# Kernel tuning notes

Hardware: AMD Instinct MI355X
Metric: run time of the kernel (lower is better)

Reference implementation:

```python
import jax, jax.numpy as jnp
import numpy as np


def setup_inputs() -> dict:
    key = jax.random.key(0)
    k1, k2, k3, k4, k5 = jax.random.split(key, 5)
    B, S, D, F, E = 4, 4096, 1024, 2048, 8
    top_k = 2
    num_tokens = B * S
    capacity = max(int(num_tokens / E * 1.25), 4)  # 2560
    scale = 0.02
    return {
        "x": jax.random.normal(k1, (B, S, D), dtype=jnp.float32),
        "gate_w": jax.random.normal(k2, (D, E), dtype=jnp.float32) * scale,
        "w_gate": jax.random.normal(k3, (E, D, F), dtype=jnp.float32) * scale,
        "w_up": jax.random.normal(k4, (E, D, F), dtype=jnp.float32) * scale,
        "w_down": jax.random.normal(k5, (E, F, D), dtype=jnp.float32) * scale,
        "num_experts": E,
        "top_k": top_k,
        "capacity": capacity,
    }


AUX_LOSS_WEIGHT = 0.01


def reference(x, gate_w, w_gate, w_up, w_down, num_experts, top_k, capacity):
    B, S, D = x.shape
    N = B * S
    x_flat = x.reshape(N, D)

    # ---- Router ----
    logits = x_flat @ gate_w                      # [N, E]
    probs = jax.nn.softmax(logits, axis=-1)
    weights, indices = jax.lax.top_k(probs, top_k)  # [N, K]
    weights = weights / jnp.sum(weights, axis=-1, keepdims=True)

    # ---- Capacity-based dispatch ----
    indices_flat = indices.reshape(-1)            # [N*K]
    x_rep = jnp.repeat(x_flat, top_k, axis=0)     # [N*K, D]
    expert_mask = jax.nn.one_hot(indices_flat, num_experts, dtype=jnp.int32)  # [N*K, E]
    token_priority = jnp.cumsum(expert_mask, axis=0) * expert_mask
    token_rank = jnp.sum(token_priority, axis=1)  # [N*K], 1-based rank within expert
    valid = (token_rank > 0) & (token_rank <= capacity)
    gather_idx = indices_flat * capacity + (token_rank - 1)  # [N*K]

    total_slots = num_experts * capacity
    # drop-mode scatter: invalid rows are sent out-of-bounds and dropped
    safe_idx = jnp.where(valid, gather_idx, total_slots)
    dispatched = jnp.zeros((total_slots, D), dtype=x.dtype)
    dispatched = dispatched.at[safe_idx].set(x_rep, mode="drop")
    dispatched = dispatched.reshape(num_experts, capacity, D)  # [E, C, D]

    # ---- Fused experts (grouped BMM, SwiGLU) ----
    gate = jnp.einsum("ecd,edf->ecf", dispatched, w_gate)
    up = jnp.einsum("ecd,edf->ecf", dispatched, w_up)
    hidden = jax.nn.silu(gate) * up
    expert_out = jnp.einsum("ecf,efd->ecd", hidden, w_down)
    expert_out_flat = expert_out.reshape(total_slots, D)

    # ---- Combine (row-aligned gather; dropped tokens contribute zero) ----
    gathered = expert_out_flat[jnp.clip(gather_idx, 0, total_slots - 1)]
    combined = jnp.where(valid[:, None], gathered, jnp.zeros((), dtype=x.dtype))
    combined = combined.reshape(N, top_k, D)
    output = jnp.sum(combined * weights[:, :, None], axis=1)  # [N, D]

    # ---- Aux load-balance loss ----
    mask = jax.nn.one_hot(indices, num_experts, dtype=jnp.float32).sum(axis=1)  # [N, E]
    f = mask.sum(axis=0) / (N * top_k + 1e-9)
    P = probs.mean(axis=0)
    aux_loss = num_experts * jnp.sum(f * P) * AUX_LOSS_WEIGHT

    return output.reshape(B, S, D), aux_loss
```

## Files before the change

kernel.cpp:

```cpp
#include <hip/hip_runtime.h>
#include <stdint.h>

#define N_TOK 16384
#define DIM   1024
#define NEXP  8
#define FF    2048
#define CAP   2560
#define NSLOT (NEXP*CAP)

using f32x4  = __attribute__((ext_vector_type(4))) float;
using bf16x8 = __attribute__((ext_vector_type(8))) short;

__device__ __forceinline__ unsigned short f2bf(float f){
  union { float f; unsigned u; } c; c.f = f;
  unsigned u = c.u + 0x7FFFu + ((c.u >> 16) & 1u);
  return (unsigned short)(u >> 16);
}
__device__ __forceinline__ float bf2f(unsigned short h){
  union { unsigned u; float f; } c; c.u = ((unsigned)h) << 16; return c.f;
}

__device__ __forceinline__ void gld16(const unsigned short* g, unsigned short* l){
  __builtin_amdgcn_global_load_lds((__attribute__((address_space(1))) void*)(void*)g,
                                   (__attribute__((address_space(3))) void*)l,
                                   16, 0, 0);
}

#define HBAR __builtin_amdgcn_s_barrier()
#define LG0  asm volatile("s_waitcnt lgkmcnt(0)" ::: "memory")

__global__ __launch_bounds__(256) void k_router(
    const float* __restrict__ x, const float* __restrict__ gate_w,
    float* __restrict__ probs, int* __restrict__ topidx, float* __restrict__ topw)
{
  __shared__ float gwT[NEXP][DIM];
  int tid = threadIdx.x;
  for (int i = tid; i < DIM*NEXP; i += 256) gwT[i & 7][i >> 3] = gate_w[i];
  __syncthreads();
  int wave = tid >> 6, lane = tid & 63;
  int t = blockIdx.x * 4 + wave;
  const float* xr = x + (size_t)t * DIM;
  double acc[NEXP];
  #pragma unroll
  for (int e = 0; e < NEXP; e++) acc[e] = 0.0;
  for (int j = 0; j < DIM/64; j++){
    double xv = (double)xr[lane + 64*j];
    #pragma unroll
    for (int e = 0; e < NEXP; e++) acc[e] += xv * (double)gwT[e][lane + 64*j];
  }
  #pragma unroll
  for (int off = 32; off >= 1; off >>= 1){
    #pragma unroll
    for (int e = 0; e < NEXP; e++) acc[e] += __shfl_xor(acc[e], off, 64);
  }
  if (lane == 0){
    double m = acc[0];
    #pragma unroll
    for (int e = 1; e < NEXP; e++) m = fmax(m, acc[e]);
    double p[NEXP], Z = 0.0;
    #pragma unroll
    for (int e = 0; e < NEXP; e++){ p[e] = exp(acc[e] - m); Z += p[e]; }
    double invZ = 1.0 / Z;
    #pragma unroll
    for (int e = 0; e < NEXP; e++){ p[e] *= invZ; probs[t*NEXP + e] = (float)p[e]; }
    int i0 = 0; double p0 = p[0];
    #pragma unroll
    for (int e = 1; e < NEXP; e++) if (p[e] > p0){ p0 = p[e]; i0 = e; }
    int i1 = (i0 == 0) ? 1 : 0; double p1 = p[i1];
    #pragma unroll
    for (int e = 0; e < NEXP; e++) if (e != i0 && p[e] > p1){ p1 = p[e]; i1 = e; }
    double s = p0 + p1;
    topidx[t*2+0] = i0; topidx[t*2+1] = i1;
    topw [t*2+0] = (float)(p0/s); topw[t*2+1] = (float)(p1/s);
  }
}

__global__ __launch_bounds__(1024) void k_scan(
    const int* __restrict__ topidx,
    int* __restrict__ slot_token, int* __restrict__ tok_slots,
    int* __restrict__ counts_total)
{
  __shared__ int sc[1024][NEXP];
  const int t = threadIdx.x;
  const int base_i = t * 32;
  int ids[32];
  #pragma unroll
  for (int j = 0; j < 32; j++) ids[j] = topidx[base_i + j];
  int b[NEXP];
  #pragma unroll
  for (int e = 0; e < NEXP; e++) b[e] = 0;
  #pragma unroll
  for (int j = 0; j < 32; j++){
    #pragma unroll
    for (int e = 0; e < NEXP; e++) if (ids[j] == e) b[e]++;
  }
  #pragma unroll
  for (int e = 0; e < NEXP; e++) sc[t][e] = b[e];
  __syncthreads();
  for (int off = 1; off < 1024; off <<= 1){
    int tmp[NEXP];
    #pragma unroll
    for (int e = 0; e < NEXP; e++) tmp[e] = (t >= off) ? sc[t-off][e] : 0;
    __syncthreads();
    #pragma unroll
    for (int e = 0; e < NEXP; e++) sc[t][e] += tmp[e];
    __syncthreads();
  }
  int myb[NEXP];
  #pragma unroll
  for (int e = 0; e < NEXP; e++) myb[e] = sc[t][e] - b[e];
  if (t == 1023){
    #pragma unroll
    for (int e = 0; e < NEXP; e++) counts_total[e] = sc[1023][e];
  }
  #pragma unroll
  for (int j = 0; j < 32; j++){
    int slot = -1;
    #pragma unroll
    for (int e = 0; e < NEXP; e++){
      if (ids[j] == e){
        int r = myb[e]; myb[e] = r + 1;
        if (r < CAP){
          slot = e*CAP + r;
          slot_token[slot] = (base_i + j) >> 1;
        }
      }
    }
    tok_slots[base_i + j] = slot;
  }
}

template<int MODE>
__global__ __launch_bounds__(256) void k_tcv(
    const float* __restrict__ in, unsigned short* __restrict__ out,
    int R, int C, size_t estride)
{
  __shared__ float tt[64][65];
  const int e  = blockIdx.z;
  const float* ine = in + (size_t)e * R * C;
  unsigned short* oute = out + (size_t)e * estride;
  const int c0 = blockIdx.x * 64, r0 = blockIdx.y * 64;
  const int tid = threadIdx.x;
  #pragma unroll
  for (int i = 0; i < 4; i++){
    int idx = i*256 + tid;
    int row = idx >> 4, c4 = idx & 15;
    float4 v = *(const float4*)(ine + (size_t)(r0 + row)*C + c0 + c4*4);
    tt[c4*4+0][row] = v.x; tt[c4*4+1][row] = v.y;
    tt[c4*4+2][row] = v.z; tt[c4*4+3][row] = v.w;
  }
  __syncthreads();
  #pragma unroll
  for (int i = 0; i < 2; i++){
    int cl = i*32 + (tid >> 3);
    int rs = (tid & 7) * 8;
    int c  = c0 + cl;
    int orow = (MODE == 0) ? ((c>>4)*32 + (c&15))
             : (MODE == 1) ? ((c>>4)*32 + 16 + (c&15))
             : c;
    unsigned long long pk0 = 0, pk1 = 0;
    #pragma unroll
    for (int j = 0; j < 4; j++) pk0 |= (unsigned long long)f2bf(tt[cl][rs+j]) << (16*j);
    #pragma unroll
    for (int j = 0; j < 4; j++) pk1 |= (unsigned long long)f2bf(tt[cl][rs+4+j]) << (16*j);
    unsigned long long* dst = (unsigned long long*)(oute + (size_t)orow*R + r0 + rs);
    dst[0] = pk0; dst[1] = pk1;
  }
}

__global__ __launch_bounds__(256) void k_gather(
    const float* __restrict__ x, const int* __restrict__ slot_token,
    unsigned short* __restrict__ disp)
{
  const int s = blockIdx.x;
  const int t = slot_token[s];
  const int tid = threadIdx.x;
  unsigned long long pk = 0ull;
  if (t >= 0){
    float4 v = *(const float4*)(x + (size_t)t*DIM + tid*4);
    pk =  (unsigned long long)f2bf(v.x)
       | ((unsigned long long)f2bf(v.y) << 16)
       | ((unsigned long long)f2bf(v.z) << 32)
       | ((unsigned long long)f2bf(v.w) << 48);
  }
  *(unsigned long long*)(disp + (size_t)s*DIM + tid*4) = pk;
}

__device__ __forceinline__ void stg(const unsigned short* gsrc, int ldg,
                                    unsigned short* Lh, int wave, int lane){
  const int sl = (lane & 3) ^ ((lane >> 3) & 3);
  #pragma unroll
  for (int j = 0; j < 2; j++){
    int bi = wave*2 + j;
    gld16(gsrc + (size_t)(bi*16 + (lane >> 2))*ldg + sl*8, Lh + bi*512);
  }
}
__device__ __forceinline__ bf16x8 frd(const unsigned short* Lh, int r, int g){
  return *(const bf16x8*)(Lh + r*32 + (((g ^ ((r >> 1) & 3))) << 3));
}
template<int MG>
__device__ __forceinline__ void mm16(f32x4 (&acc)[8][4], const bf16x8 (&a)[4], const bf16x8 (&b)[4]){
  #pragma unroll
  for (int i = 0; i < 4; i++)
    #pragma unroll
    for (int n = 0; n < 4; n++)
      acc[MG*4+i][n] = __builtin_amdgcn_mfma_f32_16x16x32_bf16(a[i], b[n], acc[MG*4+i][n], 0, 0, 0);
}

#define HALF_STEP(RS, DOSTG, VMW, ASRC, BSRC)                                   \
  {                                                                             \
    unsigned short* LA = lds + (RS)*16384;                                      \
    unsigned short* LB = LA + 8192;                                             \
    unsigned short* NS = lds + (((RS)+3)&3)*16384;                              \
    bf16x8 a[4], b[4];                                                          \
    _Pragma("unroll")                                                           \
    for (int i = 0; i < 4; i++) a[i] = frd(LA, wr*128 + i*16 + l15, g);         \
    _Pragma("unroll")                                                           \
    for (int n = 0; n < 4; n++) b[n] = frd(LB, wc*64 + n*16 + l15, g);          \
    if (DOSTG) stg(ASRC, KDIM, NS, wave, lane);                                 \
    HBAR; LG0;                                                                  \
    __builtin_amdgcn_s_setprio(1);  mm16<0>(acc, a, b);                         \
    __builtin_amdgcn_s_setprio(0);                                              \
    HBAR;                                                                       \
    _Pragma("unroll")                                                           \
    for (int i = 0; i < 4; i++) a[i] = frd(LA, wr*128 + (4+i)*16 + l15, g);     \
    if (DOSTG) stg(BSRC, KDIM, NS + 8192, wave, lane);                          \
    HBAR; LG0;                                                                  \
    __builtin_amdgcn_s_setprio(1);  mm16<1>(acc, a, b);                         \
    __builtin_amdgcn_s_setprio(0);                                              \
    if ((VMW) == 4) { asm volatile("s_waitcnt vmcnt(4)" ::: "memory"); }        \
    else if ((VMW) == 0) { asm volatile("s_waitcnt vmcnt(0)" ::: "memory"); }   \
    HBAR;                                                                       \
  }

template<int KDIM, int EPI>
__global__ __launch_bounds__(512, 2) void k_gemm8(
    const unsigned short* __restrict__ A,
    const unsigned short* __restrict__ B,
    unsigned short* __restrict__ Out)
{
  constexpr int NH    = KDIM / 32;
  constexpr int BROWS = (EPI == 1) ? 2*FF : DIM;
  constexpr int LDO   = (EPI == 1) ? FF : DIM;
  __shared__ unsigned short lds[65536];
  const int id = blockIdx.x;
  const int e  = id & 7;
  const int t  = id >> 3;
  const int mt = t % 10, nt = t / 10;
  const int m0 = mt*256, n0 = nt*256;
  const unsigned short* Ab = A + ((size_t)e*CAP   + m0) * KDIM;
  const unsigned short* Bb = B + ((size_t)e*BROWS + n0) * KDIM;
  const int tid = threadIdx.x, wave = tid >> 6, lane = tid & 63;
  const int wr = wave >> 2, wc = wave & 3;
  const int g = lane >> 4, l15 = lane & 15;

  f32x4 acc[8][4];
  const f32x4 z4 = {0.f,0.f,0.f,0.f};
  #pragma unroll
  for (int i = 0; i < 8; i++)
    #pragma unroll
    for (int n = 0; n < 4; n++) acc[i][n] = z4;

  stg(Ab,      KDIM, lds + 0*16384,        wave, lane);
  stg(Bb,      KDIM, lds + 0*16384 + 8192, wave, lane);
  stg(Ab + 32, KDIM, lds + 1*16384,        wave, lane);
  stg(Bb + 32, KDIM, lds + 1*16384 + 8192, wave, lane);
  stg(Ab + 64, KDIM, lds + 2*16384,        wave, lane);
  stg(Bb + 64, KDIM, lds + 2*16384 + 8192, wave, lane);
  asm volatile("s_waitcnt vmcnt(4)" ::: "memory");
  HBAR;

  for (int h = 0; h + 8 <= NH; h += 4){
    HALF_STEP(0, true, -1, Ab + (size_t)(h+3)*32, Bb + (size_t)(h+3)*32);
    HALF_STEP(1, true,  4, Ab + (size_t)(h+4)*32, Bb + (size_t)(h+4)*32);
    HALF_STEP(2, true, -1, Ab + (size_t)(h+5)*32, Bb + (size_t)(h+5)*32);
    HALF_STEP(3, true,  4, Ab + (size_t)(h+6)*32, Bb + (size_t)(h+6)*32);
  }
  HALF_STEP(0, true, -1, Ab + (size_t)(NH-1)*32, Bb + (size_t)(NH-1)*32);
  HALF_STEP(1, false, 0, Ab, Bb);
  HALF_STEP(2, false, -1, Ab, Bb);
  HALF_STEP(3, false, -1, Ab, Bb);

  if (EPI == 1){
    unsigned short* H = Out + ((size_t)e*CAP + m0 + wr*128) * (size_t)LDO;
    const int hc0 = (n0 + wc*64) >> 1;
    #pragma unroll
    for (int mf = 0; mf < 8; mf++)
      #pragma unroll
      for (int q = 0; q < 4; q++){
        int r = mf*16 + g*4 + q;
        #pragma unroll
        for (int p = 0; p < 2; p++){
          float gg = acc[mf][2*p][q], uu = acc[mf][2*p+1][q];
          float h = gg / (1.f + __expf(-gg)) * uu;
          H[(size_t)r*LDO + hc0 + p*16 + l15] = f2bf(h);
        }
      }
  } else {
    unsigned short* O = Out + ((size_t)e*CAP + m0 + wr*128) * (size_t)LDO + n0 + wc*64;
    #pragma unroll
    for (int mf = 0; mf < 8; mf++)
      #pragma unroll
      for (int q = 0; q < 4; q++){
        int r = mf*16 + g*4 + q;
        #pragma unroll
        for (int n = 0; n < 4; n++)
          O[(size_t)r*LDO + n*16 + l15] = f2bf(acc[mf][n][q]);
      }
  }
}

__global__ __launch_bounds__(256) void k_combine(
    const unsigned short* __restrict__ slot_out, const int* __restrict__ tok_slots,
    const float* __restrict__ topw, float* __restrict__ out)
{
  const int t = blockIdx.x*2 + (threadIdx.x >> 7);
  const int tid = threadIdx.x & 127;
  const int s0 = tok_slots[t*2+0], s1 = tok_slots[t*2+1];
  const float w0 = topw[t*2+0], w1 = topw[t*2+1];
  float r[8];
  #pragma unroll
  for (int j = 0; j < 8; j++) r[j] = 0.f;
  if (s0 >= 0){
    bf16x8 v = *(const bf16x8*)(slot_out + (size_t)s0*DIM + tid*8);
    #pragma unroll
    for (int j = 0; j < 8; j++) r[j] += w0 * bf2f((unsigned short)v[j]);
  }
  if (s1 >= 0){
    bf16x8 v = *(const bf16x8*)(slot_out + (size_t)s1*DIM + tid*8);
    #pragma unroll
    for (int j = 0; j < 8; j++) r[j] += w1 * bf2f((unsigned short)v[j]);
  }
  float4* o = (float4*)(out + (size_t)t*DIM + tid*8);
  o[0] = make_float4(r[0], r[1], r[2], r[3]);
  o[1] = make_float4(r[4], r[5], r[6], r[7]);
}

__global__ __launch_bounds__(256) void k_aux(
    const float* __restrict__ probs, const int* __restrict__ counts_total,
    float* __restrict__ aux_out)
{
  const int tid = threadIdx.x;
  float pe[NEXP];
  #pragma unroll
  for (int e = 0; e < NEXP; e++) pe[e] = 0.f;
  for (int i = tid; i < N_TOK; i += 256){
    #pragma unroll
    for (int e = 0; e < NEXP; e++) pe[e] += probs[i*NEXP + e];
  }
  #pragma unroll
  for (int off = 32; off >= 1; off >>= 1){
    #pragma unroll
    for (int e = 0; e < NEXP; e++) pe[e] += __shfl_xor(pe[e], off, 64);
  }
  __shared__ float part[4][NEXP];
  const int wave = tid >> 6, lane = tid & 63;
  if (lane == 0){
    #pragma unroll
    for (int e = 0; e < NEXP; e++) part[wave][e] = pe[e];
  }
  __syncthreads();
  if (tid == 0){
    float aux = 0.f;
    for (int e = 0; e < NEXP; e++){
      float P = (part[0][e] + part[1][e] + part[2][e] + part[3][e]) / (float)N_TOK;
      float f = (float)counts_total[e] / ((float)(N_TOK*2) + 1e-9f);
      aux += f * P;
    }
    aux_out[0] = (float)NEXP * aux * 0.01f;
  }
}

extern "C" void kernel_launch(void* const* d_in, const int* in_sizes, int n_in,
                              void* d_out, int out_size, void* d_ws, size_t ws_size,
                              hipStream_t stream)
{
  const float* x      = (const float*)d_in[0];
  const float* gate_w = (const float*)d_in[1];
  const float* w_gate = (const float*)d_in[2];
  const float* w_up   = (const float*)d_in[3];
  const float* w_down = (const float*)d_in[4];
  float* out = (float*)d_out;

  uint8_t* ws = (uint8_t*)d_ws;
  float* probs        = (float*)ws;             ws += (size_t)N_TOK*NEXP*4;
  int*   topidx       = (int*)ws;               ws += (size_t)N_TOK*2*4;
  float* topw         = (float*)ws;             ws += (size_t)N_TOK*2*4;
  int*   slot_token   = (int*)ws;               ws += (size_t)NSLOT*4;
  int*   tok_slots    = (int*)ws;               ws += (size_t)N_TOK*2*4;
  int*   counts_total = (int*)ws;               ws += 256;
  unsigned short* disp   = (unsigned short*)ws; ws += (size_t)NSLOT*DIM*2;
  unsigned short* hidden = (unsigned short*)ws; ws += (size_t)NSLOT*FF*2;
  unsigned short* B1     = (unsigned short*)ws; ws += (size_t)NEXP*2*FF*DIM*2;
  unsigned short* wdT    = (unsigned short*)ws; ws += (size_t)NEXP*DIM*FF*2;
  size_t need = (size_t)(ws - (uint8_t*)d_ws);
  if (ws_size < need) return;
  unsigned short* slot_out = disp;

  hipMemsetAsync(slot_token, 0xFF, (size_t)NSLOT * sizeof(int), stream);

  k_router<<<N_TOK/4, 256, 0, stream>>>(x, gate_w, probs, topidx, topw);
  k_scan<<<1, 1024, 0, stream>>>(topidx, slot_token, tok_slots, counts_total);
  k_tcv<0><<<dim3(FF/64, DIM/64, NEXP), 256, 0, stream>>>(w_gate, B1, DIM, FF, (size_t)2*FF*DIM);
  k_tcv<1><<<dim3(FF/64, DIM/64, NEXP), 256, 0, stream>>>(w_up,   B1, DIM, FF, (size_t)2*FF*DIM);
  k_tcv<2><<<dim3(DIM/64, FF/64, NEXP), 256, 0, stream>>>(w_down, wdT, FF, DIM, (size_t)DIM*FF);
  k_gather<<<NSLOT, 256, 0, stream>>>(x, slot_token, disp);
  k_gemm8<DIM, 1><<<1280, 512, 0, stream>>>(disp, B1, hidden);
  k_gemm8<FF, 2><<<320, 512, 0, stream>>>(hidden, wdT, slot_out);
  k_combine<<<N_TOK/2, 256, 0, stream>>>(slot_out, tok_slots, topw, out);
  k_aux<<<1, 256, 0, stream>>>(probs, counts_total, out + (size_t)N_TOK*DIM);
}
```

Baseline: 508.8 us.

## Split GEMM kernels; shrink LDS pipeline and use smaller tiles for down projection

```diff
diff --git a/kernel.cpp b/kernel.cpp
--- a/kernel.cpp
+++ b/kernel.cpp
@@ -28,6 +28,7 @@
 
 #define HBAR __builtin_amdgcn_s_barrier()
 #define LG0  asm volatile("s_waitcnt lgkmcnt(0)" ::: "memory")
+#define VM0  asm volatile("s_waitcnt vmcnt(0)" ::: "memory")
 
 __global__ __launch_bounds__(256) void k_router(
     const float* __restrict__ x, const float* __restrict__ gate_w,
@@ -207,49 +208,20 @@
       acc[MG*4+i][n] = __builtin_amdgcn_mfma_f32_16x16x32_bf16(a[i], b[n], acc[MG*4+i][n], 0, 0, 0);
 }
 
-#define HALF_STEP(RS, DOSTG, VMW, ASRC, BSRC)                                   \
-  {                                                                             \
-    unsigned short* LA = lds + (RS)*16384;                                      \
-    unsigned short* LB = LA + 8192;                                             \
-    unsigned short* NS = lds + (((RS)+3)&3)*16384;                              \
-    bf16x8 a[4], b[4];                                                          \
-    _Pragma("unroll")                                                           \
-    for (int i = 0; i < 4; i++) a[i] = frd(LA, wr*128 + i*16 + l15, g);         \
-    _Pragma("unroll")                                                           \
-    for (int n = 0; n < 4; n++) b[n] = frd(LB, wc*64 + n*16 + l15, g);          \
-    if (DOSTG) stg(ASRC, KDIM, NS, wave, lane);                                 \
-    HBAR; LG0;                                                                  \
-    __builtin_amdgcn_s_setprio(1);  mm16<0>(acc, a, b);                         \
-    __builtin_amdgcn_s_setprio(0);                                              \
-    HBAR;                                                                       \
-    _Pragma("unroll")                                                           \
-    for (int i = 0; i < 4; i++) a[i] = frd(LA, wr*128 + (4+i)*16 + l15, g);     \
-    if (DOSTG) stg(BSRC, KDIM, NS + 8192, wave, lane);                          \
-    HBAR; LG0;                                                                  \
-    __builtin_amdgcn_s_setprio(1);  mm16<1>(acc, a, b);                         \
-    __builtin_amdgcn_s_setprio(0);                                              \
-    if ((VMW) == 4) { asm volatile("s_waitcnt vmcnt(4)" ::: "memory"); }        \
-    else if ((VMW) == 0) { asm volatile("s_waitcnt vmcnt(0)" ::: "memory"); }   \
-    HBAR;                                                                       \
-  }
-
-template<int KDIM, int EPI>
-__global__ __launch_bounds__(512, 2) void k_gemm8(
+__global__ __launch_bounds__(512, 4) void k_gemm1(
     const unsigned short* __restrict__ A,
     const unsigned short* __restrict__ B,
     unsigned short* __restrict__ Out)
 {
-  constexpr int NH    = KDIM / 32;
-  constexpr int BROWS = (EPI == 1) ? 2*FF : DIM;
-  constexpr int LDO   = (EPI == 1) ? FF : DIM;
-  __shared__ unsigned short lds[65536];
+  constexpr int KDIM = DIM, NH = DIM/32;
+  __shared__ unsigned short lds[32768];
   const int id = blockIdx.x;
   const int e  = id & 7;
   const int t  = id >> 3;
   const int mt = t % 10, nt = t / 10;
   const int m0 = mt*256, n0 = nt*256;
-  const unsigned short* Ab = A + ((size_t)e*CAP   + m0) * KDIM;
-  const unsigned short* Bb = B + ((size_t)e*BROWS + n0) * KDIM;
+  const unsigned short* Ab = A + ((size_t)e*CAP  + m0) * KDIM;
+  const unsigned short* Bb = B + ((size_t)e*2*FF + n0) * KDIM;
   const int tid = threadIdx.x, wave = tid >> 6, lane = tid & 63;
   const int wr = wave >> 2, wc = wave & 3;
   const int g = lane >> 4, l15 = lane & 15;
@@ -261,53 +233,114 @@
     #pragma unroll
     for (int n = 0; n < 4; n++) acc[i][n] = z4;
 
-  stg(Ab,      KDIM, lds + 0*16384,        wave, lane);
-  stg(Bb,      KDIM, lds + 0*16384 + 8192, wave, lane);
-  stg(Ab + 32, KDIM, lds + 1*16384,        wave, lane);
-  stg(Bb + 32, KDIM, lds + 1*16384 + 8192, wave, lane);
-  stg(Ab + 64, KDIM, lds + 2*16384,        wave, lane);
-  stg(Bb + 64, KDIM, lds + 2*16384 + 8192, wave, lane);
-  asm volatile("s_waitcnt vmcnt(4)" ::: "memory");
-  HBAR;
-
-  for (int h = 0; h + 8 <= NH; h += 4){
-    HALF_STEP(0, true, -1, Ab + (size_t)(h+3)*32, Bb + (size_t)(h+3)*32);
-    HALF_STEP(1, true,  4, Ab + (size_t)(h+4)*32, Bb + (size_t)(h+4)*32);
-    HALF_STEP(2, true, -1, Ab + (size_t)(h+5)*32, Bb + (size_t)(h+5)*32);
-    HALF_STEP(3, true,  4, Ab + (size_t)(h+6)*32, Bb + (size_t)(h+6)*32);
-  }
-  HALF_STEP(0, true, -1, Ab + (size_t)(NH-1)*32, Bb + (size_t)(NH-1)*32);
-  HALF_STEP(1, false, 0, Ab, Bb);
-  HALF_STEP(2, false, -1, Ab, Bb);
-  HALF_STEP(3, false, -1, Ab, Bb);
-
-  if (EPI == 1){
-    unsigned short* H = Out + ((size_t)e*CAP + m0 + wr*128) * (size_t)LDO;
-    const int hc0 = (n0 + wc*64) >> 1;
-    #pragma unroll
-    for (int mf = 0; mf < 8; mf++)
+  stg(Ab, KDIM, lds,        wave, lane);
+  stg(Bb, KDIM, lds + 8192, wave, lane);
+  VM0; HBAR;
+
+  for (int h = 0; h < NH; ++h){
+    unsigned short* LA = lds + (h & 1)*16384;
+    unsigned short* LB = LA + 8192;
+    unsigned short* NS = lds + ((h & 1)^1)*16384;
+    const bool st = (h + 1 < NH);
+    bf16x8 a[4], b[4];
+    #pragma unroll
+    for (int i = 0; i < 4; i++) a[i] = frd(LA, wr*128 + i*16 + l15, g);
+    #pragma unroll
+    for (int n = 0; n < 4; n++) b[n] = frd(LB, wc*64 + n*16 + l15, g);
+    if (st) stg(Ab + (size_t)(h+1)*32, KDIM, NS, wave, lane);
+    HBAR; LG0;
+    __builtin_amdgcn_s_setprio(1);  mm16<0>(acc, a, b);  __builtin_amdgcn_s_setprio(0);
+    HBAR;
+    #pragma unroll
+    for (int i = 0; i < 4; i++) a[i] = frd(LA, wr*128 + (4+i)*16 + l15, g);
+    if (st) stg(Bb + (size_t)(h+1)*32, KDIM, NS + 8192, wave, lane);
+    HBAR; LG0;
+    __builtin_amdgcn_s_setprio(1);  mm16<1>(acc, a, b);  __builtin_amdgcn_s_setprio(0);
+    if (st) VM0;
+    HBAR;
+  }
+
+  unsigned short* H = Out + ((size_t)e*CAP + m0 + wr*128) * (size_t)FF;
+  const int hc0 = (n0 + wc*64) >> 1;
+  #pragma unroll
+  for (int mf = 0; mf < 8; mf++)
+    #pragma unroll
+    for (int q = 0; q < 4; q++){
+      int r = mf*16 + g*4 + q;
       #pragma unroll
-      for (int q = 0; q < 4; q++){
-        int r = mf*16 + g*4 + q;
-        #pragma unroll
-        for (int p = 0; p < 2; p++){
-          float gg = acc[mf][2*p][q], uu = acc[mf][2*p+1][q];
-          float h = gg / (1.f + __expf(-gg)) * uu;
-          H[(size_t)r*LDO + hc0 + p*16 + l15] = f2bf(h);
-        }
+      for (int p = 0; p < 2; p++){
+        float gg = acc[mf][2*p][q], uu = acc[mf][2*p+1][q];
+        float h = gg / (1.f + __expf(-gg)) * uu;
+        H[(size_t)r*FF + hc0 + p*16 + l15] = f2bf(h);
       }
-  } else {
-    unsigned short* O = Out + ((size_t)e*CAP + m0 + wr*128) * (size_t)LDO + n0 + wc*64;
-    #pragma unroll
-    for (int mf = 0; mf < 8; mf++)
+    }
+}
+
+__global__ __launch_bounds__(256, 4) void k_gemm2s(
+    const unsigned short* __restrict__ A,
+    const unsigned short* __restrict__ B,
+    unsigned short* __restrict__ Out)
+{
+  constexpr int KDIM = FF, NH = FF/32;
+  __shared__ unsigned short lds[16384];
+  const int id = blockIdx.x;
+  const int e  = id & 7;
+  const int t  = id >> 3;
+  const int mt = t % 20, nt = t / 20;
+  const int m0 = mt*128, n0 = nt*128;
+  const unsigned short* Ab = A + ((size_t)e*CAP + m0) * KDIM;
+  const unsigned short* Bb = B + ((size_t)e*DIM + n0) * KDIM;
+  const int tid = threadIdx.x, wave = tid >> 6, lane = tid & 63;
+  const int wr = wave >> 1, wc = wave & 1;
+  const int g = lane >> 4, l15 = lane & 15;
+
+  f32x4 acc[4][4];
+  const f32x4 z4 = {0.f,0.f,0.f,0.f};
+  #pragma unroll
+  for (int i = 0; i < 4; i++)
+    #pragma unroll
+    for (int n = 0; n < 4; n++) acc[i][n] = z4;
+
+  stg(Ab, KDIM, lds,        wave, lane);
+  stg(Bb, KDIM, lds + 4096, wave, lane);
+  VM0; HBAR;
+
+  for (int h = 0; h < NH; ++h){
+    unsigned short* LA = lds + (h & 1)*8192;
+    unsigned short* LB = LA + 4096;
+    unsigned short* NS = lds + ((h & 1)^1)*8192;
+    const bool st = (h + 1 < NH);
+    bf16x8 a[4], b[4];
+    #pragma unroll
+    for (int i = 0; i < 4; i++) a[i] = frd(LA, wr*64 + i*16 + l15, g);
+    #pragma unroll
+    for (int n = 0; n < 4; n++) b[n] = frd(LB, wc*64 + n*16 + l15, g);
+    if (st){
+      stg(Ab + (size_t)(h+1)*32, KDIM, NS,        wave, lane);
+      stg(Bb + (size_t)(h+1)*32, KDIM, NS + 4096, wave, lane);
+    }
+    HBAR; LG0;
+    __builtin_amdgcn_s_setprio(1);
+    #pragma unroll
+    for (int i = 0; i < 4; i++)
       #pragma unroll
-      for (int q = 0; q < 4; q++){
-        int r = mf*16 + g*4 + q;
-        #pragma unroll
-        for (int n = 0; n < 4; n++)
-          O[(size_t)r*LDO + n*16 + l15] = f2bf(acc[mf][n][q]);
-      }
-  }
+      for (int n = 0; n < 4; n++)
+        acc[i][n] = __builtin_amdgcn_mfma_f32_16x16x32_bf16(a[i], b[n], acc[i][n], 0, 0, 0);
+    __builtin_amdgcn_s_setprio(0);
+    if (st) VM0;
+    HBAR;
+  }
+
+  unsigned short* O = Out + ((size_t)e*CAP + m0 + wr*64) * (size_t)DIM + n0 + wc*64;
+  #pragma unroll
+  for (int mf = 0; mf < 4; mf++)
+    #pragma unroll
+    for (int q = 0; q < 4; q++){
+      int r = mf*16 + g*4 + q;
+      #pragma unroll
+      for (int n = 0; n < 4; n++)
+        O[(size_t)r*DIM + n*16 + l15] = f2bf(acc[mf][n][q]);
+    }
 }
 
 __global__ __launch_bounds__(256) void k_combine(
@@ -405,8 +438,8 @@
   k_tcv<1><<<dim3(FF/64, DIM/64, NEXP), 256, 0, stream>>>(w_up,   B1, DIM, FF, (size_t)2*FF*DIM);
   k_tcv<2><<<dim3(DIM/64, FF/64, NEXP), 256, 0, stream>>>(w_down, wdT, FF, DIM, (size_t)DIM*FF);
   k_gather<<<NSLOT, 256, 0, stream>>>(x, slot_token, disp);
-  k_gemm8<DIM, 1><<<1280, 512, 0, stream>>>(disp, B1, hidden);
-  k_gemm8<FF, 2><<<320, 512, 0, stream>>>(hidden, wdT, slot_out);
+  k_gemm1<<<1280, 512, 0, stream>>>(disp, B1, hidden);
+  k_gemm2s<<<1280, 256, 0, stream>>>(hidden, wdT, slot_out);
   k_combine<<<N_TOK/2, 256, 0, stream>>>(slot_out, tok_slots, topw, out);
   k_aux<<<1, 256, 0, stream>>>(probs, counts_total, out + (size_t)N_TOK*DIM);
 }
```

After: 2.032 ms. 299% more time.

## Split-K the down-projection GEMM into two partials summed in combine

Applied to the files above, without the earlier changes.

```diff
diff --git a/kernel.cpp b/kernel.cpp
--- a/kernel.cpp
+++ b/kernel.cpp
@@ -217,14 +217,14 @@
     for (int i = 0; i < 4; i++) a[i] = frd(LA, wr*128 + i*16 + l15, g);         \
     _Pragma("unroll")                                                           \
     for (int n = 0; n < 4; n++) b[n] = frd(LB, wc*64 + n*16 + l15, g);          \
-    if (DOSTG) stg(ASRC, KDIM, NS, wave, lane);                                 \
+    if (DOSTG) stg(ASRC, LDG, NS, wave, lane);                                  \
     HBAR; LG0;                                                                  \
     __builtin_amdgcn_s_setprio(1);  mm16<0>(acc, a, b);                         \
     __builtin_amdgcn_s_setprio(0);                                              \
     HBAR;                                                                       \
     _Pragma("unroll")                                                           \
     for (int i = 0; i < 4; i++) a[i] = frd(LA, wr*128 + (4+i)*16 + l15, g);     \
-    if (DOSTG) stg(BSRC, KDIM, NS + 8192, wave, lane);                          \
+    if (DOSTG) stg(BSRC, LDG, NS + 8192, wave, lane);                           \
     HBAR; LG0;                                                                  \
     __builtin_amdgcn_s_setprio(1);  mm16<1>(acc, a, b);                         \
     __builtin_amdgcn_s_setprio(0);                                              \
@@ -233,11 +233,12 @@
     HBAR;                                                                       \
   }
 
-template<int KDIM, int EPI>
+template<int KDIM, int LDG, int EPI>
 __global__ __launch_bounds__(512, 2) void k_gemm8(
     const unsigned short* __restrict__ A,
     const unsigned short* __restrict__ B,
-    unsigned short* __restrict__ Out)
+    unsigned short* __restrict__ Out0,
+    unsigned short* __restrict__ Out1)
 {
   constexpr int NH    = KDIM / 32;
   constexpr int BROWS = (EPI == 1) ? 2*FF : DIM;
@@ -245,11 +246,13 @@
   __shared__ unsigned short lds[65536];
   const int id = blockIdx.x;
   const int e  = id & 7;
-  const int t  = id >> 3;
+  int t  = id >> 3;
+  int ks = 0;
+  if (EPI == 2){ ks = t & 1; t >>= 1; }
   const int mt = t % 10, nt = t / 10;
   const int m0 = mt*256, n0 = nt*256;
-  const unsigned short* Ab = A + ((size_t)e*CAP   + m0) * KDIM;
-  const unsigned short* Bb = B + ((size_t)e*BROWS + n0) * KDIM;
+  const unsigned short* Ab = A + ((size_t)e*CAP   + m0) * LDG + (size_t)ks*KDIM;
+  const unsigned short* Bb = B + ((size_t)e*BROWS + n0) * LDG + (size_t)ks*KDIM;
   const int tid = threadIdx.x, wave = tid >> 6, lane = tid & 63;
   const int wr = wave >> 2, wc = wave & 3;
   const int g = lane >> 4, l15 = lane & 15;
@@ -261,12 +264,12 @@
     #pragma unroll
     for (int n = 0; n < 4; n++) acc[i][n] = z4;
 
-  stg(Ab,      KDIM, lds + 0*16384,        wave, lane);
-  stg(Bb,      KDIM, lds + 0*16384 + 8192, wave, lane);
-  stg(Ab + 32, KDIM, lds + 1*16384,        wave, lane);
-  stg(Bb + 32, KDIM, lds + 1*16384 + 8192, wave, lane);
-  stg(Ab + 64, KDIM, lds + 2*16384,        wave, lane);
-  stg(Bb + 64, KDIM, lds + 2*16384 + 8192, wave, lane);
+  stg(Ab,      LDG, lds + 0*16384,        wave, lane);
+  stg(Bb,      LDG, lds + 0*16384 + 8192, wave, lane);
+  stg(Ab + 32, LDG, lds + 1*16384,        wave, lane);
+  stg(Bb + 32, LDG, lds + 1*16384 + 8192, wave, lane);
+  stg(Ab + 64, LDG, lds + 2*16384,        wave, lane);
+  stg(Bb + 64, LDG, lds + 2*16384 + 8192, wave, lane);
   asm volatile("s_waitcnt vmcnt(4)" ::: "memory");
   HBAR;
 
@@ -282,7 +285,7 @@
   HALF_STEP(3, false, -1, Ab, Bb);
 
   if (EPI == 1){
-    unsigned short* H = Out + ((size_t)e*CAP + m0 + wr*128) * (size_t)LDO;
+    unsigned short* H = Out0 + ((size_t)e*CAP + m0 + wr*128) * (size_t)LDO;
     const int hc0 = (n0 + wc*64) >> 1;
     #pragma unroll
     for (int mf = 0; mf < 8; mf++)
@@ -297,7 +300,8 @@
         }
       }
   } else {
-    unsigned short* O = Out + ((size_t)e*CAP + m0 + wr*128) * (size_t)LDO + n0 + wc*64;
+    unsigned short* P = (ks ? Out1 : Out0);
+    unsigned short* O = P + ((size_t)e*CAP + m0 + wr*128) * (size_t)LDO + n0 + wc*64;
     #pragma unroll
     for (int mf = 0; mf < 8; mf++)
       #pragma unroll
@@ -311,8 +315,9 @@
 }
 
 __global__ __launch_bounds__(256) void k_combine(
-    const unsigned short* __restrict__ slot_out, const int* __restrict__ tok_slots,
-    const float* __restrict__ topw, float* __restrict__ out)
+    const unsigned short* __restrict__ P0, const unsigned short* __restrict__ P1,
+    const int* __restrict__ tok_slots, const float* __restrict__ topw,
+    float* __restrict__ out)
 {
   const int t = blockIdx.x*2 + (threadIdx.x >> 7);
   const int tid = threadIdx.x & 127;
@@ -322,14 +327,18 @@
   #pragma unroll
   for (int j = 0; j < 8; j++) r[j] = 0.f;
   if (s0 >= 0){
-    bf16x8 v = *(const bf16x8*)(slot_out + (size_t)s0*DIM + tid*8);
-    #pragma unroll
-    for (int j = 0; j < 8; j++) r[j] += w0 * bf2f((unsigned short)v[j]);
+    bf16x8 v0 = *(const bf16x8*)(P0 + (size_t)s0*DIM + tid*8);
+    bf16x8 v1 = *(const bf16x8*)(P1 + (size_t)s0*DIM + tid*8);
+    #pragma unroll
+    for (int j = 0; j < 8; j++)
+      r[j] += w0 * (bf2f((unsigned short)v0[j]) + bf2f((unsigned short)v1[j]));
   }
   if (s1 >= 0){
-    bf16x8 v = *(const bf16x8*)(slot_out + (size_t)s1*DIM + tid*8);
-    #pragma unroll
-    for (int j = 0; j < 8; j++) r[j] += w1 * bf2f((unsigned short)v[j]);
+    bf16x8 v0 = *(const bf16x8*)(P0 + (size_t)s1*DIM + tid*8);
+    bf16x8 v1 = *(const bf16x8*)(P1 + (size_t)s1*DIM + tid*8);
+    #pragma unroll
+    for (int j = 0; j < 8; j++)
+      r[j] += w1 * (bf2f((unsigned short)v0[j]) + bf2f((unsigned short)v1[j]));
   }
   float4* o = (float4*)(out + (size_t)t*DIM + tid*8);
   o[0] = make_float4(r[0], r[1], r[2], r[3]);
@@ -395,7 +404,8 @@
   unsigned short* wdT    = (unsigned short*)ws; ws += (size_t)NEXP*DIM*FF*2;
   size_t need = (size_t)(ws - (uint8_t*)d_ws);
   if (ws_size < need) return;
-  unsigned short* slot_out = disp;
+  unsigned short* P0 = disp;
+  unsigned short* P1 = B1;
 
   hipMemsetAsync(slot_token, 0xFF, (size_t)NSLOT * sizeof(int), stream);
 
@@ -405,8 +415,8 @@
   k_tcv<1><<<dim3(FF/64, DIM/64, NEXP), 256, 0, stream>>>(w_up,   B1, DIM, FF, (size_t)2*FF*DIM);
   k_tcv<2><<<dim3(DIM/64, FF/64, NEXP), 256, 0, stream>>>(w_down, wdT, FF, DIM, (size_t)DIM*FF);
   k_gather<<<NSLOT, 256, 0, stream>>>(x, slot_token, disp);
-  k_gemm8<DIM, 1><<<1280, 512, 0, stream>>>(disp, B1, hidden);
-  k_gemm8<FF, 2><<<320, 512, 0, stream>>>(hidden, wdT, slot_out);
-  k_combine<<<N_TOK/2, 256, 0, stream>>>(slot_out, tok_slots, topw, out);
+  k_gemm8<DIM, DIM, 1><<<1280, 512, 0, stream>>>(disp, B1, hidden, nullptr);
+  k_gemm8<DIM, FF, 2><<<640, 512, 0, stream>>>(hidden, wdT, P0, P1);
+  k_combine<<<N_TOK/2, 256, 0, stream>>>(P0, P1, tok_slots, topw, out);
   k_aux<<<1, 256, 0, stream>>>(probs, counts_total, out + (size_t)N_TOK*DIM);
 }
```

Result: no change. 501.6 us (-1.4%).

## Split down-projection GEMM into a narrower-tile kernel with its own pipeline

Applied to the files above, without the earlier changes.

```diff
diff --git a/kernel.cpp b/kernel.cpp
--- a/kernel.cpp
+++ b/kernel.cpp
@@ -28,6 +28,7 @@
 
 #define HBAR __builtin_amdgcn_s_barrier()
 #define LG0  asm volatile("s_waitcnt lgkmcnt(0)" ::: "memory")
+#define SBAR0 __builtin_amdgcn_sched_barrier(0)
 
 __global__ __launch_bounds__(256) void k_router(
     const float* __restrict__ x, const float* __restrict__ gate_w,
@@ -233,23 +234,20 @@
     HBAR;                                                                       \
   }
 
-template<int KDIM, int EPI>
-__global__ __launch_bounds__(512, 2) void k_gemm8(
+__global__ __launch_bounds__(512, 2) void k_gemm1(
     const unsigned short* __restrict__ A,
     const unsigned short* __restrict__ B,
     unsigned short* __restrict__ Out)
 {
-  constexpr int NH    = KDIM / 32;
-  constexpr int BROWS = (EPI == 1) ? 2*FF : DIM;
-  constexpr int LDO   = (EPI == 1) ? FF : DIM;
+  constexpr int KDIM = DIM, NH = DIM/32;
   __shared__ unsigned short lds[65536];
   const int id = blockIdx.x;
   const int e  = id & 7;
   const int t  = id >> 3;
   const int mt = t % 10, nt = t / 10;
   const int m0 = mt*256, n0 = nt*256;
-  const unsigned short* Ab = A + ((size_t)e*CAP   + m0) * KDIM;
-  const unsigned short* Bb = B + ((size_t)e*BROWS + n0) * KDIM;
+  const unsigned short* Ab = A + ((size_t)e*CAP  + m0) * KDIM;
+  const unsigned short* Bb = B + ((size_t)e*2*FF + n0) * KDIM;
   const int tid = threadIdx.x, wave = tid >> 6, lane = tid & 63;
   const int wr = wave >> 2, wc = wave & 3;
   const int g = lane >> 4, l15 = lane & 15;
@@ -281,33 +279,103 @@
   HALF_STEP(2, false, -1, Ab, Bb);
   HALF_STEP(3, false, -1, Ab, Bb);
 
-  if (EPI == 1){
-    unsigned short* H = Out + ((size_t)e*CAP + m0 + wr*128) * (size_t)LDO;
-    const int hc0 = (n0 + wc*64) >> 1;
-    #pragma unroll
-    for (int mf = 0; mf < 8; mf++)
+  unsigned short* H = Out + ((size_t)e*CAP + m0 + wr*128) * (size_t)FF;
+  const int hc0 = (n0 + wc*64) >> 1;
+  #pragma unroll
+  for (int mf = 0; mf < 8; mf++)
+    #pragma unroll
+    for (int q = 0; q < 4; q++){
+      int r = mf*16 + g*4 + q;
       #pragma unroll
-      for (int q = 0; q < 4; q++){
-        int r = mf*16 + g*4 + q;
-        #pragma unroll
-        for (int p = 0; p < 2; p++){
-          float gg = acc[mf][2*p][q], uu = acc[mf][2*p+1][q];
-          float h = gg / (1.f + __expf(-gg)) * uu;
-          H[(size_t)r*LDO + hc0 + p*16 + l15] = f2bf(h);
-        }
+      for (int p = 0; p < 2; p++){
+        float gg = acc[mf][2*p][q], uu = acc[mf][2*p+1][q];
+        float h = gg / (1.f + __expf(-gg)) * uu;
+        H[(size_t)r*FF + hc0 + p*16 + l15] = f2bf(h);
       }
-  } else {
-    unsigned short* O = Out + ((size_t)e*CAP + m0 + wr*128) * (size_t)LDO + n0 + wc*64;
-    #pragma unroll
-    for (int mf = 0; mf < 8; mf++)
+    }
+}
+
+__global__ __launch_bounds__(512, 2) void k_gemm2t(
+    const unsigned short* __restrict__ A,
+    const unsigned short* __restrict__ B,
+    unsigned short* __restrict__ Out)
+{
+  constexpr int KDIM = FF, NH = FF/32;
+  constexpr int SLOT = 12288;
+  __shared__ unsigned short lds[4*SLOT];
+  const int id = blockIdx.x;
+  const int e  = id & 7;
+  const int t  = id >> 3;
+  const int mt = t % 10, nt = t / 10;
+  const int m0 = mt*256, n0 = nt*128;
+  const unsigned short* Ab = A + ((size_t)e*CAP + m0) * KDIM;
+  const unsigned short* Bb = B + ((size_t)e*DIM + n0) * KDIM;
+  const int tid = threadIdx.x, wave = tid >> 6, lane = tid & 63;
+  const int wr = wave >> 2, wc = wave & 3;
+  const int g = lane >> 4, l15 = lane & 15;
+  const int sl = (lane & 3) ^ ((lane >> 3) & 3);
+
+  f32x4 acc[8][2];
+  const f32x4 z4 = {0.f,0.f,0.f,0.f};
+  #pragma unroll
+  for (int i = 0; i < 8; i++)
+    #pragma unroll
+    for (int n = 0; n < 2; n++) acc[i][n] = z4;
+
+  auto stage = [&](int h, int rs){
+    unsigned short* S = lds + rs*SLOT;
+    const unsigned short* As = Ab + (size_t)h*32;
+    const unsigned short* Bs = Bb + (size_t)h*32;
+    #pragma unroll
+    for (int j = 0; j < 2; j++){
+      int bi = wave*2 + j;
+      gld16(As + (size_t)(bi*16 + (lane >> 2))*KDIM + sl*8, S + bi*512);
+    }
+    gld16(Bs + (size_t)(wave*16 + (lane >> 2))*KDIM + sl*8, S + 8192 + wave*512);
+  };
+
+  stage(0,0); stage(1,1); stage(2,2);
+
+  for (int h = 0; h < NH; ++h){
+    if (h < NH-2)      { asm volatile("s_waitcnt vmcnt(6)" ::: "memory"); }
+    else if (h == NH-2){ asm volatile("s_waitcnt vmcnt(3)" ::: "memory"); }
+    else               { asm volatile("s_waitcnt vmcnt(0)" ::: "memory"); }
+    HBAR;
+    SBAR0;
+    unsigned short* LA = lds + (h & 3)*SLOT;
+    unsigned short* LB = LA + 8192;
+    if (h + 3 < NH) stage(h+3, (h+3) & 3);
+    bf16x8 a[4], a2[4], b[2];
+    #pragma unroll
+    for (int i = 0; i < 4; i++) a[i]  = frd(LA, wr*128 + i*16 + l15, g);
+    #pragma unroll
+    for (int n = 0; n < 2; n++) b[n]  = frd(LB, wc*32 + n*16 + l15, g);
+    #pragma unroll
+    for (int i = 0; i < 4; i++) a2[i] = frd(LA, wr*128 + (4+i)*16 + l15, g);
+    __builtin_amdgcn_s_setprio(1);
+    #pragma unroll
+    for (int i = 0; i < 4; i++)
       #pragma unroll
-      for (int q = 0; q < 4; q++){
-        int r = mf*16 + g*4 + q;
-        #pragma unroll
-        for (int n = 0; n < 4; n++)
-          O[(size_t)r*LDO + n*16 + l15] = f2bf(acc[mf][n][q]);
-      }
-  }
+      for (int n = 0; n < 2; n++)
+        acc[i][n] = __builtin_amdgcn_mfma_f32_16x16x32_bf16(a[i], b[n], acc[i][n], 0, 0, 0);
+    #pragma unroll
+    for (int i = 0; i < 4; i++)
+      #pragma unroll
+      for (int n = 0; n < 2; n++)
+        acc[4+i][n] = __builtin_amdgcn_mfma_f32_16x16x32_bf16(a2[i], b[n], acc[4+i][n], 0, 0, 0);
+    __builtin_amdgcn_s_setprio(0);
+  }
+
+  unsigned short* O = Out + ((size_t)e*CAP + m0 + wr*128) * (size_t)DIM + n0 + wc*32;
+  #pragma unroll
+  for (int mf = 0; mf < 8; mf++)
+    #pragma unroll
+    for (int q = 0; q < 4; q++){
+      int r = mf*16 + g*4 + q;
+      #pragma unroll
+      for (int n = 0; n < 2; n++)
+        O[(size_t)r*DIM + n*16 + l15] = f2bf(acc[mf][n][q]);
+    }
 }
 
 __global__ __launch_bounds__(256) void k_combine(
@@ -405,8 +473,8 @@
   k_tcv<1><<<dim3(FF/64, DIM/64, NEXP), 256, 0, stream>>>(w_up,   B1, DIM, FF, (size_t)2*FF*DIM);
   k_tcv<2><<<dim3(DIM/64, FF/64, NEXP), 256, 0, stream>>>(w_down, wdT, FF, DIM, (size_t)DIM*FF);
   k_gather<<<NSLOT, 256, 0, stream>>>(x, slot_token, disp);
-  k_gemm8<DIM, 1><<<1280, 512, 0, stream>>>(disp, B1, hidden);
-  k_gemm8<FF, 2><<<320, 512, 0, stream>>>(hidden, wdT, slot_out);
+  k_gemm1<<<1280, 512, 0, stream>>>(disp, B1, hidden);
+  k_gemm2t<<<640, 512, 0, stream>>>(hidden, wdT, slot_out);
   k_combine<<<N_TOK/2, 256, 0, stream>>>(slot_out, tok_slots, topw, out);
   k_aux<<<1, 256, 0, stream>>>(probs, counts_total, out + (size_t)N_TOK*DIM);
 }
```

Result: no change. 517.2 us (+1.7%).
